# Kernel tuning notes

Hardware: AMD Instinct MI355X
Metric: run time of the kernel (lower is better)

## Reference

```python
import jax, jax.numpy as jnp
import numpy as np

D_MODEL = 1024
NUM_HEADS = 16
D_K = D_MODEL // NUM_HEADS
B, S = 2, 2048


def setup_inputs() -> dict:
    key = jax.random.key(0)
    ks = jax.random.split(key, 4)
    scale = 1.0 / np.sqrt(D_MODEL)
    x = jax.random.normal(ks[0], (B, S, D_MODEL), dtype=jnp.float32)
    w_qkv = jax.random.normal(ks[1], (D_MODEL, 3 * D_MODEL), dtype=jnp.float32) * scale
    b_qkv = jnp.zeros((3 * D_MODEL,), dtype=jnp.float32)
    w_out = jax.random.normal(ks[2], (D_MODEL, D_MODEL), dtype=jnp.float32) * scale
    b_out = jnp.zeros((D_MODEL,), dtype=jnp.float32)
    # causal mask: 1 where attention is allowed (j <= i), 0 elsewhere
    mask = jnp.tril(jnp.ones((S, S), dtype=jnp.int32))
    return {"x": x, "mask": mask, "w_qkv": w_qkv, "b_qkv": b_qkv,
            "w_out": w_out, "b_out": b_out}


def reference(x, mask, w_qkv, b_qkv, w_out, b_out):
    Bb, Ss, C = x.shape
    qkv = x @ w_qkv + b_qkv                      # [B,S,3C]
    q, k, v = jnp.split(qkv, 3, axis=-1)
    def split_heads(t):
        return t.reshape(Bb, Ss, NUM_HEADS, D_K).transpose(0, 2, 1, 3)  # [B,H,S,Dk]
    q, k, v = split_heads(q), split_heads(k), split_heads(v)
    scores = jnp.einsum('bhqd,bhkd->bhqk', q, k) / jnp.sqrt(jnp.float32(D_K))
    scores = jnp.where(mask == 0, -jnp.inf, scores)
    weights = jax.nn.softmax(scores, axis=-1)
    weights = jnp.nan_to_num(weights, nan=0.0)   # matches torch.nan_to_num
    attn = jnp.einsum('bhqk,bhkd->bhqd', weights, v)
    attn = attn.transpose(0, 2, 1, 3).reshape(Bb, Ss, C)
    return attn @ w_out + b_out
```

## Files before the change

kernel.cpp:

```cpp
#include <hip/hip_runtime.h>
#include <hip/hip_bf16.h>

#define D_MODEL 1024
#define NUM_HEADS 16
#define D_K 64
#define BATCH 2
#define SEQ 2048

typedef __attribute__((ext_vector_type(8))) short bf16x8;
typedef __attribute__((ext_vector_type(4))) float f32x4;

union P16 { int4 i4; ushort u[8]; };
union FU { float f; unsigned int u; };

__device__ __forceinline__ float bf2f(ushort u) {
    union { unsigned int i; float f; } c; c.i = ((unsigned int)u) << 16; return c.f;
}
__device__ __forceinline__ ushort f2bf(float f) {
    union { float f; unsigned int i; } c; c.f = f;
    unsigned int x = c.i;
    return (ushort)((x + 0x7fff + ((x >> 16) & 1)) >> 16);
}

__device__ __forceinline__ bool wave_detect_f32(const ushort* x) {
    ushort u = x[2 * (threadIdx.x & 63)];
    int e = (u >> 7) & 0xFF;
    unsigned long long bl = __ballot(e >= 100 && e <= 141);
    return __popcll(bl) < 32;
}

__global__ __launch_bounds__(256)
void prep_all(const ushort* __restrict__ x, const void* __restrict__ Wq,
              const void* __restrict__ Wo, ushort* __restrict__ xb,
              ushort* __restrict__ WqT, ushort* __restrict__ WoT,
              int* __restrict__ flag)
{
    const bool f32 = wave_detect_f32(x);
    const int bx = blockIdx.x, tx = threadIdx.x;
    if (bx == 0 && tx == 0) flag[0] = f32 ? 1 : 0;

    if (bx >= 1024) {
        if (!f32) return;
        int i = ((bx - 1024) * 256 + tx) * 8;
        const float* f = (const float*)x + i;
        float4 a = *(const float4*)f, b = *(const float4*)(f + 4);
        P16 r;
        r.u[0] = f2bf(a.x); r.u[1] = f2bf(a.y); r.u[2] = f2bf(a.z); r.u[3] = f2bf(a.w);
        r.u[4] = f2bf(b.x); r.u[5] = f2bf(b.y); r.u[6] = f2bf(b.z); r.u[7] = f2bf(b.w);
        *(int4*)(xb + i) = r.i4;
        return;
    }

    __shared__ ushort t[64][72];
    const int nb = bx & 63, kb = bx >> 6;
    const void* W; ushort* WT; int N, n0;
    if (nb < 48) { W = Wq; WT = WqT; N = 3 * D_MODEL; n0 = nb * 64; }
    else         { W = Wo; WT = WoT; N = D_MODEL;     n0 = (nb - 48) * 64; }
    const int k0 = kb * 64, K = D_MODEL;
    #pragma unroll
    for (int p = 0; p < 16; ++p) {
        int r = p * 4 + (tx >> 6), c = tx & 63;
        float v = f32 ? ((const float*)W)[(size_t)(k0 + r) * N + n0 + c]
                      : bf2f(((const ushort*)W)[(size_t)(k0 + r) * N + n0 + c]);
        t[r][c] = f2bf(v);
    }
    __syncthreads();
    #pragma unroll
    for (int p = 0; p < 16; ++p) {
        int nn = p * 4 + (tx >> 6), kk = tx & 63;
        WT[(size_t)(n0 + nn) * K + k0 + kk] = t[kk][nn];
    }
}

template<int MODE>
__global__ __launch_bounds__(256)
void gemm128(const void* __restrict__ Araw, const ushort* __restrict__ Aconv,
             const ushort* __restrict__ WT, const void* __restrict__ bias,
             void* __restrict__ out, int N, int K, const int* __restrict__ flag)
{
    __shared__ ushort As[2][128 * 32];
    __shared__ ushort Bs[2][128 * 32];

    const int f = *flag;
    const ushort* A = (MODE == 1) ? (f ? Aconv : (const ushort*)Araw) : Aconv;

    const int tid = threadIdx.x;
    const int w = tid >> 6, lane = tid & 63;
    const int ln = lane & 15, quad = lane >> 4;
    const int m0 = blockIdx.y * 128, n0 = blockIdx.x * 128;
    const int wm = (w >> 1) * 64, wn = (w & 1) * 64;

    const int s0 = w * 128 + lane, s1 = s0 + 64;
    const int ar0 = s0 >> 2, ak0 = ((s0 & 3) ^ ((ar0 >> 1) & 3)) * 8;
    const int ar1 = s1 >> 2, ak1 = ((s1 & 3) ^ ((ar1 >> 1) & 3)) * 8;
    const size_t aoff0 = (size_t)(m0 + ar0) * K + ak0;
    const size_t aoff1 = (size_t)(m0 + ar1) * K + ak1;
    const size_t boff0 = (size_t)(n0 + ar0) * K + ak0;
    const size_t boff1 = (size_t)(n0 + ar1) * K + ak1;

    const int physc = (quad ^ ((ln >> 1) & 3)) * 8;

    f32x4 acc[4][4] = {};

    const int nk = K >> 5;
    int4 a0 = *(const int4*)(A + aoff0);
    int4 a1 = *(const int4*)(A + aoff1);
    int4 b0 = *(const int4*)(WT + boff0);
    int4 b1 = *(const int4*)(WT + boff1);
    *(int4*)(As[0] + s0 * 8) = a0;
    *(int4*)(As[0] + s1 * 8) = a1;
    *(int4*)(Bs[0] + s0 * 8) = b0;
    *(int4*)(Bs[0] + s1 * 8) = b1;
    a0 = *(const int4*)(A + aoff0 + 32);
    a1 = *(const int4*)(A + aoff1 + 32);
    b0 = *(const int4*)(WT + boff0 + 32);
    b1 = *(const int4*)(WT + boff1 + 32);
    __syncthreads();

    for (int kt = 0; kt < nk; ++kt) {
        const int cur = kt & 1;
        if (kt + 1 < nk) {
            *(int4*)(As[1 - cur] + s0 * 8) = a0;
            *(int4*)(As[1 - cur] + s1 * 8) = a1;
            *(int4*)(Bs[1 - cur] + s0 * 8) = b0;
            *(int4*)(Bs[1 - cur] + s1 * 8) = b1;
        }
        if (kt + 2 < nk) {
            const int kc = (kt + 2) * 32;
            a0 = *(const int4*)(A + aoff0 + kc);
            a1 = *(const int4*)(A + aoff1 + kc);
            b0 = *(const int4*)(WT + boff0 + kc);
            b1 = *(const int4*)(WT + boff1 + kc);
        }

        bf16x8 af[4], bf[4];
        #pragma unroll
        for (int t = 0; t < 4; ++t) {
            af[t] = *(const bf16x8*)(As[cur] + (wm + t * 16 + ln) * 32 + physc);
            bf[t] = *(const bf16x8*)(Bs[cur] + (wn + t * 16 + ln) * 32 + physc);
        }
        #pragma unroll
        for (int mi = 0; mi < 4; ++mi)
            #pragma unroll
            for (int ni = 0; ni < 4; ++ni)
                acc[mi][ni] = __builtin_amdgcn_mfma_f32_16x16x32_bf16(
                    af[mi], bf[ni], acc[mi][ni], 0, 0, 0);
        __syncthreads();
    }

    #pragma unroll
    for (int mi = 0; mi < 4; ++mi) {
        #pragma unroll
        for (int ni = 0; ni < 4; ++ni) {
            int col = n0 + wn + ni * 16 + ln;
            float bb = f ? ((const float*)bias)[col] : bf2f(((const ushort*)bias)[col]);
            #pragma unroll
            for (int r = 0; r < 4; ++r) {
                int row = m0 + wm + mi * 16 + quad * 4 + r;
                float v = acc[mi][ni][r] + bb;
                if (MODE == 0 && f) ((float*)out)[(size_t)row * N + col] = v;
                else                ((ushort*)out)[(size_t)row * N + col] = f2bf(v);
            }
        }
    }
}

template<int MODE>
__global__ __launch_bounds__(256)
void gemm64(const void* __restrict__ Araw, const ushort* __restrict__ Aconv,
            const ushort* __restrict__ WT, const void* __restrict__ bias,
            void* __restrict__ out, int N, int K, const int* __restrict__ flag)
{
    __shared__ ushort As[2][64 * 32];
    __shared__ ushort Bs[2][128 * 32];

    const int f = *flag;
    const ushort* A = (MODE == 1) ? (f ? Aconv : (const ushort*)Araw) : Aconv;

    const int tid = threadIdx.x;
    const int w = tid >> 6, lane = tid & 63;
    const int ln = lane & 15, quad = lane >> 4;
    const int m0 = blockIdx.y * 64, n0 = blockIdx.x * 128;
    const int wn = w * 32;

    const int sa = tid;
    const int arow = sa >> 2, akc = ((sa & 3) ^ ((arow >> 1) & 3)) * 8;
    const size_t aoff = (size_t)(m0 + arow) * K + akc;
    const int sb0 = tid, sb1 = tid + 256;
    const int br0 = sb0 >> 2, bk0 = ((sb0 & 3) ^ ((br0 >> 1) & 3)) * 8;
    const int br1 = sb1 >> 2, bk1 = ((sb1 & 3) ^ ((br1 >> 1) & 3)) * 8;
    const size_t boff0 = (size_t)(n0 + br0) * K + bk0;
    const size_t boff1 = (size_t)(n0 + br1) * K + bk1;

    const int physc = (quad ^ ((ln >> 1) & 3)) * 8;

    f32x4 acc[4][2] = {};

    const int nk = K >> 5;
    int4 a0 = *(const int4*)(A + aoff);
    int4 b0 = *(const int4*)(WT + boff0);
    int4 b1 = *(const int4*)(WT + boff1);
    *(int4*)(As[0] + sa * 8)  = a0;
    *(int4*)(Bs[0] + sb0 * 8) = b0;
    *(int4*)(Bs[0] + sb1 * 8) = b1;
    a0 = *(const int4*)(A + aoff + 32);
    b0 = *(const int4*)(WT + boff0 + 32);
    b1 = *(const int4*)(WT + boff1 + 32);
    __syncthreads();

    for (int kt = 0; kt < nk; ++kt) {
        const int cur = kt & 1;
        if (kt + 1 < nk) {
            *(int4*)(As[1 - cur] + sa * 8)  = a0;
            *(int4*)(Bs[1 - cur] + sb0 * 8) = b0;
            *(int4*)(Bs[1 - cur] + sb1 * 8) = b1;
        }
        if (kt + 2 < nk) {
            const int kc = (kt + 2) * 32;
            a0 = *(const int4*)(A + aoff + kc);
            b0 = *(const int4*)(WT + boff0 + kc);
            b1 = *(const int4*)(WT + boff1 + kc);
        }

        bf16x8 af[4], bf[2];
        #pragma unroll
        for (int t = 0; t < 4; ++t)
            af[t] = *(const bf16x8*)(As[cur] + (t * 16 + ln) * 32 + physc);
        #pragma unroll
        for (int t = 0; t < 2; ++t)
            bf[t] = *(const bf16x8*)(Bs[cur] + (wn + t * 16 + ln) * 32 + physc);
        #pragma unroll
        for (int mi = 0; mi < 4; ++mi)
            #pragma unroll
            for (int ni = 0; ni < 2; ++ni)
                acc[mi][ni] = __builtin_amdgcn_mfma_f32_16x16x32_bf16(
                    af[mi], bf[ni], acc[mi][ni], 0, 0, 0);
        __syncthreads();
    }

    #pragma unroll
    for (int mi = 0; mi < 4; ++mi) {
        #pragma unroll
        for (int ni = 0; ni < 2; ++ni) {
            int col = n0 + wn + ni * 16 + ln;
            float bb = f ? ((const float*)bias)[col] : bf2f(((const ushort*)bias)[col]);
            #pragma unroll
            for (int r = 0; r < 4; ++r) {
                int row = m0 + mi * 16 + quad * 4 + r;
                float v = acc[mi][ni][r] + bb;
                if (MODE == 0 && f) ((float*)out)[(size_t)row * N + col] = v;
                else                ((ushort*)out)[(size_t)row * N + col] = f2bf(v);
            }
        }
    }
}

__global__ __launch_bounds__(256)
void flash_attn7(const ushort* __restrict__ qkv, ushort* __restrict__ attn)
{
    __shared__ ushort Ks[64][72];
    __shared__ ushort Vs[64][72];
    __shared__ ushort QPs[128][72];

    const int tid  = threadIdx.x;
    const int wave = tid >> 6, lane = tid & 63;
    const int ln   = lane & 15, quad = lane >> 4;
    const int pg   = wave >> 1, ww = wave & 1;
    const int bh   = blockIdx.x;
    const int ky   = blockIdx.y;
    const int k    = (ky < 8) ? ky : 23 - ky;
    const int xx   = 2 * k + pg;
    const int b    = bh >> 4, hh = bh & (NUM_HEADS - 1);
    const int W3   = 3 * D_MODEL;
    const size_t hbase = (size_t)b * SEQ * W3 + hh * D_K;

    const int q0A = 32 * (63 - xx), q0B = 32 * xx;
    const int ntA = 32 - k, ntB = k + 1;

    const int qrr = tid >> 1, qcol = (tid & 1) * 32;
    const int ksr = tid >> 2, ksc = (tid & 3) * 16;
    const int vp  = tid & 31, vg = (tid >> 5) * 8;

    {
        const int qpg = qrr >> 6, qmt = (qrr >> 5) & 1, ql = qrr & 31;
        const int qxx = 2 * k + qpg;
        const int grow = qmt ? (32 * qxx + ql) : (32 * (63 - qxx) + ql);
        const ushort* src = qkv + hbase + (size_t)grow * W3 + qcol;
        #pragma unroll
        for (int h = 0; h < 4; ++h) {
            P16 v; v.i4 = *(const int4*)(src + h * 8);
            #pragma unroll
            for (int e = 0; e < 8; ++e) v.u[e] = f2bf(bf2f(v.u[e]) * 0.18033688011f);
            *(int4*)(&QPs[qrr][qcol + h * 8]) = v.i4;
        }
    }
    __syncthreads();
    bf16x8 qf[2][2];
    #pragma unroll
    for (int mt = 0; mt < 2; ++mt)
        #pragma unroll
        for (int s = 0; s < 2; ++s)
            qf[mt][s] = *(const bf16x8*)(&QPs[pg * 64 + mt * 32 + ww * 16 + ln][s * 32 + quad * 8]);

    f32x4 acc_o[2][4] = {};
    f32x4 acc_l[2] = {};

    bf16x8 ones8;
    #pragma unroll
    for (int e = 0; e < 8; ++e) ones8[e] = (short)0x3F80;

    const ushort* Kbase = qkv + hbase + D_MODEL;
    const ushort* Vbase = qkv + hbase + 2 * D_MODEL;

    int4 kreg[2], vreg[2];
    {
        const ushort* ksrc = Kbase + (size_t)ksr * W3 + ksc;
        kreg[0] = *(const int4*)(ksrc);
        kreg[1] = *(const int4*)(ksrc + 8);
        vreg[0] = *(const int4*)(Vbase + (size_t)(2 * vp)     * W3 + vg);
        vreg[1] = *(const int4*)(Vbase + (size_t)(2 * vp + 1) * W3 + vg);
    }

    for (int jt = 0; jt < ntA; ++jt) {
        const int j0 = jt * 64;
        const bool doB = (jt < ntB);
        __syncthreads();

        *(int4*)(&Ks[ksr][ksc])     = kreg[0];
        *(int4*)(&Ks[ksr][ksc + 8]) = kreg[1];
        {
            P16 v0, v1; v0.i4 = vreg[0]; v1.i4 = vreg[1];
            #pragma unroll
            for (int e = 0; e < 8; ++e) {
                unsigned int pack = (unsigned int)v0.u[e] | ((unsigned int)v1.u[e] << 16);
                *(unsigned int*)(&Vs[vg + e][2 * vp]) = pack;
            }
        }
        __syncthreads();

        if (jt + 1 < ntA) {
            const int jn = j0 + 64;
            const ushort* ksrc = Kbase + (size_t)(jn + ksr) * W3 + ksc;
            kreg[0] = *(const int4*)(ksrc);
            kreg[1] = *(const int4*)(ksrc + 8);
            vreg[0] = *(const int4*)(Vbase + (size_t)(jn + 2 * vp)     * W3 + vg);
            vreg[1] = *(const int4*)(Vbase + (size_t)(jn + 2 * vp + 1) * W3 + vg);
        }

        f32x4 sa[2][4];
        #pragma unroll
        for (int t = 0; t < 4; ++t) {
            bf16x8 k0 = *(const bf16x8*)(&Ks[t * 16 + ln][quad * 8]);
            bf16x8 k1 = *(const bf16x8*)(&Ks[t * 16 + ln][32 + quad * 8]);
            {
                f32x4 z = {};
                z = __builtin_amdgcn_mfma_f32_16x16x32_bf16(qf[0][0], k0, z, 0, 0, 0);
                z = __builtin_amdgcn_mfma_f32_16x16x32_bf16(qf[0][1], k1, z, 0, 0, 0);
                sa[0][t] = z;
            }
            if (doB) {
                f32x4 z = {};
                z = __builtin_amdgcn_mfma_f32_16x16x32_bf16(qf[1][0], k0, z, 0, 0, 0);
                z = __builtin_amdgcn_mfma_f32_16x16x32_bf16(qf[1][1], k1, z, 0, 0, 0);
                sa[1][t] = z;
            }
        }

        if (jt == ntA - 1) {
            const int rowb = q0A + ww * 16 + quad * 4;
            #pragma unroll
            for (int t = 0; t < 4; ++t)
                #pragma unroll
                for (int r = 0; r < 4; ++r)
                    if (j0 + t * 16 + ln > rowb + r) sa[0][t][r] = -1e30f;
        }
        if (doB && jt == ntB - 1) {
            const int rowb = q0B + ww * 16 + quad * 4;
            #pragma unroll
            for (int t = 0; t < 4; ++t)
                #pragma unroll
                for (int r = 0; r < 4; ++r)
                    if (j0 + t * 16 + ln > rowb + r) sa[1][t][r] = -1e30f;
        }

        const int lnx = ln ^ ((quad & 1) * 8);
        #pragma unroll
        for (int mt = 0; mt < 2; ++mt) {
            if (mt && !doB) break;
            #pragma unroll
            for (int r = 0; r < 4; ++r) {
                const int prow = pg * 64 + mt * 32 + ww * 16 + quad * 4 + r;
                #pragma unroll
                for (int t = 0; t < 4; ++t) {
                    FU cc; cc.f = exp2f(sa[mt][t][r]);
                    QPs[prow][((t ^ (quad >> 1)) * 16) + lnx] = (ushort)(cc.u >> 16);
                }
            }
        }

        #pragma unroll
        for (int s = 0; s < 2; ++s) {
            const int pcol = s * 32 + ((quad ^ ((ln >> 2) & 3)) * 8);
            bf16x8 pf0 = *(const bf16x8*)(&QPs[pg * 64 + ww * 16 + ln][pcol]);
            bf16x8 pf1;
            if (doB) pf1 = *(const bf16x8*)(&QPs[pg * 64 + 32 + ww * 16 + ln][pcol]);
            #pragma unroll
            for (int t = 0; t < 4; ++t) {
                bf16x8 vf = *(const bf16x8*)(&Vs[t * 16 + ln][s * 32 + quad * 8]);
                acc_o[0][t] = __builtin_amdgcn_mfma_f32_16x16x32_bf16(pf0, vf, acc_o[0][t], 0, 0, 0);
                if (doB)
                    acc_o[1][t] = __builtin_amdgcn_mfma_f32_16x16x32_bf16(pf1, vf, acc_o[1][t], 0, 0, 0);
            }
            acc_l[0] = __builtin_amdgcn_mfma_f32_16x16x32_bf16(pf0, ones8, acc_l[0], 0, 0, 0);
            if (doB)
                acc_l[1] = __builtin_amdgcn_mfma_f32_16x16x32_bf16(pf1, ones8, acc_l[1], 0, 0, 0);
        }
    }

    #pragma unroll
    for (int mt = 0; mt < 2; ++mt) {
        const int q0 = mt ? q0B : q0A;
        #pragma unroll
        for (int r = 0; r < 4; ++r) {
            float inv = 1.0f / acc_l[mt][r];
            int i = q0 + ww * 16 + quad * 4 + r;
            size_t rowoff = ((size_t)(b * SEQ + i)) * D_MODEL + hh * D_K;
            #pragma unroll
            for (int t = 0; t < 4; ++t)
                attn[rowoff + t * 16 + ln] = f2bf(acc_o[mt][t][r] * inv);
        }
    }
}

extern "C" void kernel_launch(void* const* d_in, const int* in_sizes, int n_in,
                              void* d_out, int out_size, void* d_ws, size_t ws_size,
                              hipStream_t stream)
{
    const void* x     = d_in[0];
    const void* w_qkv = d_in[2];
    const void* b_qkv = d_in[3];
    const void* w_out = d_in[4];
    const void* b_out = d_in[5];

    char* ws = (char*)d_ws;
    int*    flag   = (int*)ws;                  size_t off = 256;
    ushort* WqkvT  = (ushort*)(ws + off);       off += (size_t)3 * D_MODEL * D_MODEL * 2;
    ushort* WoutT  = (ushort*)(ws + off);       off += (size_t)D_MODEL * D_MODEL * 2;
    ushort* qkv_ws = (ushort*)(ws + off);       off += (size_t)BATCH * SEQ * 3 * D_MODEL * 2;
    ushort* xb     = (ushort*)(ws + off);
    ushort* attn_ws = xb;

    const int M = BATCH * SEQ;

    prep_all<<<3072, 256, 0, stream>>>((const ushort*)x, w_qkv, w_out,
                                       xb, WqkvT, WoutT, flag);

    gemm128<1><<<dim3(3 * D_MODEL / 128, M / 128), 256, 0, stream>>>(
        x, xb, WqkvT, b_qkv, qkv_ws, 3 * D_MODEL, D_MODEL, flag);

    dim3 ga(BATCH * NUM_HEADS, 16);
    flash_attn7<<<ga, 256, 0, stream>>>(qkv_ws, attn_ws);

    gemm64<0><<<dim3(D_MODEL / 128, M / 64), 256, 0, stream>>>(
        attn_ws, attn_ws, WoutT, b_out, d_out, D_MODEL, D_MODEL, flag);
}
```

Before: 214.2 us.

## Split attention key tiles across wave pairs and double the attention grid

Each attention block now handles one pair of query tiles rather than two. Its four waves split each 64-key tile so that each wave pair computes half of the score columns and the matching half of the PV products. The partial output and row-sum accumulators are reduced through shared memory at the end. This doubles the number of blocks, aiming for better occupancy and load spread across CUs, and it adds a final cross-wave reduction plus extra barriers.

```diff
diff --git a/kernel.cpp b/kernel.cpp
--- a/kernel.cpp
+++ b/kernel.cpp
@@ -256,38 +256,36 @@
 }
 
 __global__ __launch_bounds__(256)
-void flash_attn7(const ushort* __restrict__ qkv, ushort* __restrict__ attn)
+void flash_attn8(const ushort* __restrict__ qkv, ushort* __restrict__ attn)
 {
-    __shared__ ushort Ks[64][72];
-    __shared__ ushort Vs[64][72];
-    __shared__ ushort QPs[128][72];
+    __shared__ ushort SMEM[3 * 64 * 72];
+    ushort (*Ks)[72]  = (ushort(*)[72])(SMEM);
+    ushort (*Vs)[72]  = (ushort(*)[72])(SMEM + 64 * 72);
+    ushort (*QPs)[72] = (ushort(*)[72])(SMEM + 2 * 64 * 72);
 
     const int tid  = threadIdx.x;
     const int wave = tid >> 6, lane = tid & 63;
     const int ln   = lane & 15, quad = lane >> 4;
-    const int pg   = wave >> 1, ww = wave & 1;
+    const int ww   = wave & 1;
+    const int kw   = wave >> 1;
     const int bh   = blockIdx.x;
-    const int ky   = blockIdx.y;
-    const int k    = (ky < 8) ? ky : 23 - ky;
-    const int xx   = 2 * k + pg;
+    const int xx   = blockIdx.y;
     const int b    = bh >> 4, hh = bh & (NUM_HEADS - 1);
     const int W3   = 3 * D_MODEL;
     const size_t hbase = (size_t)b * SEQ * W3 + hh * D_K;
 
     const int q0A = 32 * (63 - xx), q0B = 32 * xx;
-    const int ntA = 32 - k, ntB = k + 1;
-
-    const int qrr = tid >> 1, qcol = (tid & 1) * 32;
+    const int ntA = (65 - xx) >> 1, ntB = (xx + 2) >> 1;
+
     const int ksr = tid >> 2, ksc = (tid & 3) * 16;
     const int vp  = tid & 31, vg = (tid >> 5) * 8;
 
     {
-        const int qpg = qrr >> 6, qmt = (qrr >> 5) & 1, ql = qrr & 31;
-        const int qxx = 2 * k + qpg;
-        const int grow = qmt ? (32 * qxx + ql) : (32 * (63 - qxx) + ql);
+        const int qrr = tid >> 2, qcol = (tid & 3) * 16;
+        const int grow = (qrr < 32) ? (q0A + qrr) : (q0B + (qrr - 32));
         const ushort* src = qkv + hbase + (size_t)grow * W3 + qcol;
         #pragma unroll
-        for (int h = 0; h < 4; ++h) {
+        for (int h = 0; h < 2; ++h) {
             P16 v; v.i4 = *(const int4*)(src + h * 8);
             #pragma unroll
             for (int e = 0; e < 8; ++e) v.u[e] = f2bf(bf2f(v.u[e]) * 0.18033688011f);
@@ -300,7 +298,7 @@
     for (int mt = 0; mt < 2; ++mt)
         #pragma unroll
         for (int s = 0; s < 2; ++s)
-            qf[mt][s] = *(const bf16x8*)(&QPs[pg * 64 + mt * 32 + ww * 16 + ln][s * 32 + quad * 8]);
+            qf[mt][s] = *(const bf16x8*)(&QPs[mt * 32 + ww * 16 + ln][s * 32 + quad * 8]);
 
     f32x4 acc_o[2][4] = {};
     f32x4 acc_l[2] = {};
@@ -347,40 +345,41 @@
             vreg[1] = *(const int4*)(Vbase + (size_t)(jn + 2 * vp + 1) * W3 + vg);
         }
 
-        f32x4 sa[2][4];
-        #pragma unroll
-        for (int t = 0; t < 4; ++t) {
+        f32x4 sa[2][2];
+        #pragma unroll
+        for (int tt = 0; tt < 2; ++tt) {
+            const int t = 2 * kw + tt;
             bf16x8 k0 = *(const bf16x8*)(&Ks[t * 16 + ln][quad * 8]);
             bf16x8 k1 = *(const bf16x8*)(&Ks[t * 16 + ln][32 + quad * 8]);
             {
                 f32x4 z = {};
                 z = __builtin_amdgcn_mfma_f32_16x16x32_bf16(qf[0][0], k0, z, 0, 0, 0);
                 z = __builtin_amdgcn_mfma_f32_16x16x32_bf16(qf[0][1], k1, z, 0, 0, 0);
-                sa[0][t] = z;
+                sa[0][tt] = z;
             }
             if (doB) {
                 f32x4 z = {};
                 z = __builtin_amdgcn_mfma_f32_16x16x32_bf16(qf[1][0], k0, z, 0, 0, 0);
                 z = __builtin_amdgcn_mfma_f32_16x16x32_bf16(qf[1][1], k1, z, 0, 0, 0);
-                sa[1][t] = z;
+                sa[1][tt] = z;
             }
         }
 
         if (jt == ntA - 1) {
             const int rowb = q0A + ww * 16 + quad * 4;
             #pragma unroll
-            for (int t = 0; t < 4; ++t)
+            for (int tt = 0; tt < 2; ++tt)
                 #pragma unroll
                 for (int r = 0; r < 4; ++r)
-                    if (j0 + t * 16 + ln > rowb + r) sa[0][t][r] = -1e30f;
+                    if (j0 + (2 * kw + tt) * 16 + ln > rowb + r) sa[0][tt][r] = -1e30f;
         }
         if (doB && jt == ntB - 1) {
             const int rowb = q0B + ww * 16 + quad * 4;
             #pragma unroll
-            for (int t = 0; t < 4; ++t)
+            for (int tt = 0; tt < 2; ++tt)
                 #pragma unroll
                 for (int r = 0; r < 4; ++r)
-                    if (j0 + t * 16 + ln > rowb + r) sa[1][t][r] = -1e30f;
+                    if (j0 + (2 * kw + tt) * 16 + ln > rowb + r) sa[1][tt][r] = -1e30f;
         }
 
         const int lnx = ln ^ ((quad & 1) * 8);
@@ -389,21 +388,22 @@
             if (mt && !doB) break;
             #pragma unroll
             for (int r = 0; r < 4; ++r) {
-                const int prow = pg * 64 + mt * 32 + ww * 16 + quad * 4 + r;
-                #pragma unroll
-                for (int t = 0; t < 4; ++t) {
-                    FU cc; cc.f = exp2f(sa[mt][t][r]);
+                const int prow = mt * 32 + ww * 16 + quad * 4 + r;
+                #pragma unroll
+                for (int tt = 0; tt < 2; ++tt) {
+                    const int t = 2 * kw + tt;
+                    FU cc; cc.f = exp2f(sa[mt][tt][r]);
                     QPs[prow][((t ^ (quad >> 1)) * 16) + lnx] = (ushort)(cc.u >> 16);
                 }
             }
         }
 
-        #pragma unroll
-        for (int s = 0; s < 2; ++s) {
+        {
+            const int s = kw;
             const int pcol = s * 32 + ((quad ^ ((ln >> 2) & 3)) * 8);
-            bf16x8 pf0 = *(const bf16x8*)(&QPs[pg * 64 + ww * 16 + ln][pcol]);
+            bf16x8 pf0 = *(const bf16x8*)(&QPs[ww * 16 + ln][pcol]);
             bf16x8 pf1;
-            if (doB) pf1 = *(const bf16x8*)(&QPs[pg * 64 + 32 + ww * 16 + ln][pcol]);
+            if (doB) pf1 = *(const bf16x8*)(&QPs[32 + ww * 16 + ln][pcol]);
             #pragma unroll
             for (int t = 0; t < 4; ++t) {
                 bf16x8 vf = *(const bf16x8*)(&Vs[t * 16 + ln][s * 32 + quad * 8]);
@@ -417,17 +417,49 @@
         }
     }
 
-    #pragma unroll
-    for (int mt = 0; mt < 2; ++mt) {
-        const int q0 = mt ? q0B : q0A;
-        #pragma unroll
-        for (int r = 0; r < 4; ++r) {
-            float inv = 1.0f / acc_l[mt][r];
-            int i = q0 + ww * 16 + quad * 4 + r;
-            size_t rowoff = ((size_t)(b * SEQ + i)) * D_MODEL + hh * D_K;
+    __syncthreads();
+    float* red = (float*)SMEM;
+    if (kw == 1) {
+        float* dst = red + (ww * 64 + lane) * 41;
+        int idx = 0;
+        #pragma unroll
+        for (int mt = 0; mt < 2; ++mt)
             #pragma unroll
             for (int t = 0; t < 4; ++t)
-                attn[rowoff + t * 16 + ln] = f2bf(acc_o[mt][t][r] * inv);
+                #pragma unroll
+                for (int r = 0; r < 4; ++r) dst[idx++] = acc_o[mt][t][r];
+        #pragma unroll
+        for (int mt = 0; mt < 2; ++mt)
+            #pragma unroll
+            for (int r = 0; r < 4; ++r) dst[32 + mt * 4 + r] = acc_l[mt][r];
+    }
+    __syncthreads();
+    if (kw == 0) {
+        const float* src = red + (ww * 64 + lane) * 41;
+        int idx = 0;
+        #pragma unroll
+        for (int mt = 0; mt < 2; ++mt)
+            #pragma unroll
+            for (int t = 0; t < 4; ++t)
+                #pragma unroll
+                for (int r = 0; r < 4; ++r) acc_o[mt][t][r] += src[idx++];
+        #pragma unroll
+        for (int mt = 0; mt < 2; ++mt)
+            #pragma unroll
+            for (int r = 0; r < 4; ++r) acc_l[mt][r] += src[32 + mt * 4 + r];
+
+        #pragma unroll
+        for (int mt = 0; mt < 2; ++mt) {
+            const int q0 = mt ? q0B : q0A;
+            #pragma unroll
+            for (int r = 0; r < 4; ++r) {
+                float inv = 1.0f / acc_l[mt][r];
+                int i = q0 + ww * 16 + quad * 4 + r;
+                size_t rowoff = ((size_t)(b * SEQ + i)) * D_MODEL + hh * D_K;
+                #pragma unroll
+                for (int t = 0; t < 4; ++t)
+                    attn[rowoff + t * 16 + ln] = f2bf(acc_o[mt][t][r] * inv);
+            }
         }
     }
 }
@@ -458,8 +490,8 @@
     gemm128<1><<<dim3(3 * D_MODEL / 128, M / 128), 256, 0, stream>>>(
         x, xb, WqkvT, b_qkv, qkv_ws, 3 * D_MODEL, D_MODEL, flag);
 
-    dim3 ga(BATCH * NUM_HEADS, 16);
-    flash_attn7<<<ga, 256, 0, stream>>>(qkv_ws, attn_ws);
+    dim3 ga(BATCH * NUM_HEADS, 32);
+    flash_attn8<<<ga, 256, 0, stream>>>(qkv_ws, attn_ws);
 
     gemm64<0><<<dim3(D_MODEL / 128, M / 64), 256, 0, stream>>>(
         attn_ws, attn_ws, WoutT, b_out, d_out, D_MODEL, D_MODEL, flag);
```

Result: slower. 249.7 us (+16.6%).

## Double-buffer K/V tiles in LDS in the flash attention loop

Applied to the files above, without the earlier changes.

The attention kernel now keeps two LDS buffers for the K and V tiles. Tile 0 is written before the loop, and each iteration stores the next tile into the other buffer while computing on the current one. Global loads are issued two tiles ahead. This cuts the barriers per key tile from two to one, so LDS stores can overlap the MFMA work. The cost is more shared memory (about 55KB per block) and an extra prologue.

```diff
diff --git a/kernel.cpp b/kernel.cpp
--- a/kernel.cpp
+++ b/kernel.cpp
@@ -256,10 +256,10 @@
 }
 
 __global__ __launch_bounds__(256)
-void flash_attn7(const ushort* __restrict__ qkv, ushort* __restrict__ attn)
+void flash_attn9(const ushort* __restrict__ qkv, ushort* __restrict__ attn)
 {
-    __shared__ ushort Ks[64][72];
-    __shared__ ushort Vs[64][72];
+    __shared__ ushort Ks[2][64][72];
+    __shared__ ushort Vs[2][64][72];
     __shared__ ushort QPs[128][72];
 
     const int tid  = threadIdx.x;
@@ -320,26 +320,42 @@
         vreg[0] = *(const int4*)(Vbase + (size_t)(2 * vp)     * W3 + vg);
         vreg[1] = *(const int4*)(Vbase + (size_t)(2 * vp + 1) * W3 + vg);
     }
+    *(int4*)(&Ks[0][ksr][ksc])     = kreg[0];
+    *(int4*)(&Ks[0][ksr][ksc + 8]) = kreg[1];
+    {
+        P16 v0, v1; v0.i4 = vreg[0]; v1.i4 = vreg[1];
+        #pragma unroll
+        for (int e = 0; e < 8; ++e) {
+            unsigned int pack = (unsigned int)v0.u[e] | ((unsigned int)v1.u[e] << 16);
+            *(unsigned int*)(&Vs[0][vg + e][2 * vp]) = pack;
+        }
+    }
+    if (ntA > 1) {
+        const ushort* ksrc = Kbase + (size_t)(64 + ksr) * W3 + ksc;
+        kreg[0] = *(const int4*)(ksrc);
+        kreg[1] = *(const int4*)(ksrc + 8);
+        vreg[0] = *(const int4*)(Vbase + (size_t)(64 + 2 * vp)     * W3 + vg);
+        vreg[1] = *(const int4*)(Vbase + (size_t)(64 + 2 * vp + 1) * W3 + vg);
+    }
+    __syncthreads();
 
     for (int jt = 0; jt < ntA; ++jt) {
+        const int cur = jt & 1;
         const int j0 = jt * 64;
         const bool doB = (jt < ntB);
-        __syncthreads();
-
-        *(int4*)(&Ks[ksr][ksc])     = kreg[0];
-        *(int4*)(&Ks[ksr][ksc + 8]) = kreg[1];
-        {
+
+        if (jt + 1 < ntA) {
+            *(int4*)(&Ks[1 - cur][ksr][ksc])     = kreg[0];
+            *(int4*)(&Ks[1 - cur][ksr][ksc + 8]) = kreg[1];
             P16 v0, v1; v0.i4 = vreg[0]; v1.i4 = vreg[1];
             #pragma unroll
             for (int e = 0; e < 8; ++e) {
                 unsigned int pack = (unsigned int)v0.u[e] | ((unsigned int)v1.u[e] << 16);
-                *(unsigned int*)(&Vs[vg + e][2 * vp]) = pack;
-            }
-        }
-        __syncthreads();
-
-        if (jt + 1 < ntA) {
-            const int jn = j0 + 64;
+                *(unsigned int*)(&Vs[1 - cur][vg + e][2 * vp]) = pack;
+            }
+        }
+        if (jt + 2 < ntA) {
+            const int jn = j0 + 128;
             const ushort* ksrc = Kbase + (size_t)(jn + ksr) * W3 + ksc;
             kreg[0] = *(const int4*)(ksrc);
             kreg[1] = *(const int4*)(ksrc + 8);
@@ -350,8 +366,8 @@
         f32x4 sa[2][4];
         #pragma unroll
         for (int t = 0; t < 4; ++t) {
-            bf16x8 k0 = *(const bf16x8*)(&Ks[t * 16 + ln][quad * 8]);
-            bf16x8 k1 = *(const bf16x8*)(&Ks[t * 16 + ln][32 + quad * 8]);
+            bf16x8 k0 = *(const bf16x8*)(&Ks[cur][t * 16 + ln][quad * 8]);
+            bf16x8 k1 = *(const bf16x8*)(&Ks[cur][t * 16 + ln][32 + quad * 8]);
             {
                 f32x4 z = {};
                 z = __builtin_amdgcn_mfma_f32_16x16x32_bf16(qf[0][0], k0, z, 0, 0, 0);
@@ -406,7 +422,7 @@
             if (doB) pf1 = *(const bf16x8*)(&QPs[pg * 64 + 32 + ww * 16 + ln][pcol]);
             #pragma unroll
             for (int t = 0; t < 4; ++t) {
-                bf16x8 vf = *(const bf16x8*)(&Vs[t * 16 + ln][s * 32 + quad * 8]);
+                bf16x8 vf = *(const bf16x8*)(&Vs[cur][t * 16 + ln][s * 32 + quad * 8]);
                 acc_o[0][t] = __builtin_amdgcn_mfma_f32_16x16x32_bf16(pf0, vf, acc_o[0][t], 0, 0, 0);
                 if (doB)
                     acc_o[1][t] = __builtin_amdgcn_mfma_f32_16x16x32_bf16(pf1, vf, acc_o[1][t], 0, 0, 0);
@@ -415,6 +431,8 @@
             if (doB)
                 acc_l[1] = __builtin_amdgcn_mfma_f32_16x16x32_bf16(pf1, ones8, acc_l[1], 0, 0, 0);
         }
+
+        __syncthreads();
     }
 
     #pragma unroll
@@ -459,7 +477,7 @@
         x, xb, WqkvT, b_qkv, qkv_ws, 3 * D_MODEL, D_MODEL, flag);
 
     dim3 ga(BATCH * NUM_HEADS, 16);
-    flash_attn7<<<ga, 256, 0, stream>>>(qkv_ws, attn_ws);
+    flash_attn9<<<ga, 256, 0, stream>>>(qkv_ws, attn_ws);
 
     gemm64<0><<<dim3(D_MODEL / 128, M / 64), 256, 0, stream>>>(
         attn_ws, attn_ws, WoutT, b_out, d_out, D_MODEL, D_MODEL, flag);
```

Result: slower. 220.9 us (+3.2%).

## Split attention KV loop across two blocks and merge partials in output GEMM

Applied to the files above, without the earlier changes.

Attention now launches twice as many blocks. Each handles alternating KV tiles for its query rows and writes unnormalized fp32 partial outputs and row sums to workspace. The output projection GEMM reads both partials, adds them, normalizes, converts to bf16 while loading its A tiles, then multiplies. This raises parallelism in the attention stage and drops its normalization epilogue, at the cost of extra fp32 workspace traffic and a fallback path when the workspace is too small.

```diff
diff --git a/kernel.cpp b/kernel.cpp
--- a/kernel.cpp
+++ b/kernel.cpp
@@ -168,6 +168,7 @@
 template<int MODE>
 __global__ __launch_bounds__(256)
 void gemm64(const void* __restrict__ Araw, const ushort* __restrict__ Aconv,
+            const float* __restrict__ pL,
             const ushort* __restrict__ WT, const void* __restrict__ bias,
             void* __restrict__ out, int N, int K, const int* __restrict__ flag)
 {
@@ -175,7 +176,11 @@
     __shared__ ushort Bs[2][128 * 32];
 
     const int f = *flag;
-    const ushort* A = (MODE == 1) ? (f ? Aconv : (const ushort*)Araw) : Aconv;
+    const ushort* A = (MODE == 1) ? (f ? Aconv : (const ushort*)Araw)
+                                  : (const ushort*)Aconv;
+    const float* PO = (const float*)Araw;
+    constexpr size_t HALF_O = (size_t)BATCH * SEQ * D_MODEL;
+    constexpr size_t HALF_L = (size_t)BATCH * SEQ * NUM_HEADS;
 
     const int tid = threadIdx.x;
     const int w = tid >> 6, lane = tid & 63;
@@ -186,6 +191,7 @@
     const int sa = tid;
     const int arow = sa >> 2, akc = ((sa & 3) ^ ((arow >> 1) & 3)) * 8;
     const size_t aoff = (size_t)(m0 + arow) * K + akc;
+    const int rowl = (m0 + arow) * NUM_HEADS;
     const int sb0 = tid, sb1 = tid + 256;
     const int br0 = sb0 >> 2, bk0 = ((sb0 & 3) ^ ((br0 >> 1) & 3)) * 8;
     const int br1 = sb1 >> 2, bk1 = ((sb1 & 3) ^ ((br1 >> 1) & 3)) * 8;
@@ -197,13 +203,45 @@
     f32x4 acc[4][2] = {};
 
     const int nk = K >> 5;
-    int4 a0 = *(const int4*)(A + aoff);
+    int4 a0;
+    float4 ax0, ax1, ay0, ay1;
+
+    auto cvtA = [&](int ktile) -> int4 {
+        float il = 1.0f / (pL[rowl + (ktile >> 1)] + pL[HALF_L + rowl + (ktile >> 1)]);
+        P16 r;
+        r.u[0] = f2bf((ax0.x + ay0.x) * il);
+        r.u[1] = f2bf((ax0.y + ay0.y) * il);
+        r.u[2] = f2bf((ax0.z + ay0.z) * il);
+        r.u[3] = f2bf((ax0.w + ay0.w) * il);
+        r.u[4] = f2bf((ax1.x + ay1.x) * il);
+        r.u[5] = f2bf((ax1.y + ay1.y) * il);
+        r.u[6] = f2bf((ax1.z + ay1.z) * il);
+        r.u[7] = f2bf((ax1.w + ay1.w) * il);
+        return r.i4;
+    };
+
+    if constexpr (MODE == 2) {
+        ax0 = *(const float4*)(PO + aoff);
+        ax1 = *(const float4*)(PO + aoff + 4);
+        ay0 = *(const float4*)(PO + HALF_O + aoff);
+        ay1 = *(const float4*)(PO + HALF_O + aoff + 4);
+    } else {
+        a0 = *(const int4*)(A + aoff);
+    }
     int4 b0 = *(const int4*)(WT + boff0);
     int4 b1 = *(const int4*)(WT + boff1);
-    *(int4*)(As[0] + sa * 8)  = a0;
+    if constexpr (MODE == 2) *(int4*)(As[0] + sa * 8) = cvtA(0);
+    else                     *(int4*)(As[0] + sa * 8) = a0;
     *(int4*)(Bs[0] + sb0 * 8) = b0;
     *(int4*)(Bs[0] + sb1 * 8) = b1;
-    a0 = *(const int4*)(A + aoff + 32);
+    if constexpr (MODE == 2) {
+        ax0 = *(const float4*)(PO + aoff + 32);
+        ax1 = *(const float4*)(PO + aoff + 36);
+        ay0 = *(const float4*)(PO + HALF_O + aoff + 32);
+        ay1 = *(const float4*)(PO + HALF_O + aoff + 36);
+    } else {
+        a0 = *(const int4*)(A + aoff + 32);
+    }
     b0 = *(const int4*)(WT + boff0 + 32);
     b1 = *(const int4*)(WT + boff1 + 32);
     __syncthreads();
@@ -211,13 +249,21 @@
     for (int kt = 0; kt < nk; ++kt) {
         const int cur = kt & 1;
         if (kt + 1 < nk) {
-            *(int4*)(As[1 - cur] + sa * 8)  = a0;
+            if constexpr (MODE == 2) *(int4*)(As[1 - cur] + sa * 8) = cvtA(kt + 1);
+            else                     *(int4*)(As[1 - cur] + sa * 8) = a0;
             *(int4*)(Bs[1 - cur] + sb0 * 8) = b0;
             *(int4*)(Bs[1 - cur] + sb1 * 8) = b1;
         }
         if (kt + 2 < nk) {
             const int kc = (kt + 2) * 32;
-            a0 = *(const int4*)(A + aoff + kc);
+            if constexpr (MODE == 2) {
+                ax0 = *(const float4*)(PO + aoff + kc);
+                ax1 = *(const float4*)(PO + aoff + kc + 4);
+                ay0 = *(const float4*)(PO + HALF_O + aoff + kc);
+                ay1 = *(const float4*)(PO + HALF_O + aoff + kc + 4);
+            } else {
+                a0 = *(const int4*)(A + aoff + kc);
+            }
             b0 = *(const int4*)(WT + boff0 + kc);
             b1 = *(const int4*)(WT + boff1 + kc);
         }
@@ -248,7 +294,7 @@
             for (int r = 0; r < 4; ++r) {
                 int row = m0 + mi * 16 + quad * 4 + r;
                 float v = acc[mi][ni][r] + bb;
-                if (MODE == 0 && f) ((float*)out)[(size_t)row * N + col] = v;
+                if (MODE != 1 && f) ((float*)out)[(size_t)row * N + col] = v;
                 else                ((ushort*)out)[(size_t)row * N + col] = f2bf(v);
             }
         }
@@ -432,6 +478,189 @@
     }
 }
 
+__global__ __launch_bounds__(256)
+void flash_attn10(const ushort* __restrict__ qkv, float* __restrict__ pO,
+                  float* __restrict__ pL)
+{
+    __shared__ ushort Ks[64][72];
+    __shared__ ushort Vs[64][72];
+    __shared__ ushort QPs[128][72];
+
+    const int tid  = threadIdx.x;
+    const int wave = tid >> 6, lane = tid & 63;
+    const int ln   = lane & 15, quad = lane >> 4;
+    const int pg   = wave >> 1, ww = wave & 1;
+    const int bh   = blockIdx.x;
+    const int yy   = blockIdx.y;
+    const int ky   = yy >> 1, half = yy & 1;
+    const int k    = (ky < 8) ? ky : 23 - ky;
+    const int xx   = 2 * k + pg;
+    const int b    = bh >> 4, hh = bh & (NUM_HEADS - 1);
+    const int W3   = 3 * D_MODEL;
+    const size_t hbase = (size_t)b * SEQ * W3 + hh * D_K;
+
+    const int q0A = 32 * (63 - xx), q0B = 32 * xx;
+    const int ntA = 32 - k, ntB = k + 1;
+
+    const int qrr = tid >> 1, qcol = (tid & 1) * 32;
+    const int ksr = tid >> 2, ksc = (tid & 3) * 16;
+    const int vp  = tid & 31, vg = (tid >> 5) * 8;
+
+    {
+        const int qpg = qrr >> 6, qmt = (qrr >> 5) & 1, ql = qrr & 31;
+        const int qxx = 2 * k + qpg;
+        const int grow = qmt ? (32 * qxx + ql) : (32 * (63 - qxx) + ql);
+        const ushort* src = qkv + hbase + (size_t)grow * W3 + qcol;
+        #pragma unroll
+        for (int h = 0; h < 4; ++h) {
+            P16 v; v.i4 = *(const int4*)(src + h * 8);
+            #pragma unroll
+            for (int e = 0; e < 8; ++e) v.u[e] = f2bf(bf2f(v.u[e]) * 0.18033688011f);
+            *(int4*)(&QPs[qrr][qcol + h * 8]) = v.i4;
+        }
+    }
+    __syncthreads();
+    bf16x8 qf[2][2];
+    #pragma unroll
+    for (int mt = 0; mt < 2; ++mt)
+        #pragma unroll
+        for (int s = 0; s < 2; ++s)
+            qf[mt][s] = *(const bf16x8*)(&QPs[pg * 64 + mt * 32 + ww * 16 + ln][s * 32 + quad * 8]);
+
+    f32x4 acc_o[2][4] = {};
+    f32x4 acc_l[2] = {};
+
+    bf16x8 ones8;
+    #pragma unroll
+    for (int e = 0; e < 8; ++e) ones8[e] = (short)0x3F80;
+
+    const ushort* Kbase = qkv + hbase + D_MODEL;
+    const ushort* Vbase = qkv + hbase + 2 * D_MODEL;
+
+    int4 kreg[2], vreg[2];
+    {
+        const int jf = half * 64;
+        const ushort* ksrc = Kbase + (size_t)(jf + ksr) * W3 + ksc;
+        kreg[0] = *(const int4*)(ksrc);
+        kreg[1] = *(const int4*)(ksrc + 8);
+        vreg[0] = *(const int4*)(Vbase + (size_t)(jf + 2 * vp)     * W3 + vg);
+        vreg[1] = *(const int4*)(Vbase + (size_t)(jf + 2 * vp + 1) * W3 + vg);
+    }
+
+    for (int jt = half; jt < ntA; jt += 2) {
+        const int j0 = jt * 64;
+        const bool doB = (jt < ntB);
+        __syncthreads();
+
+        *(int4*)(&Ks[ksr][ksc])     = kreg[0];
+        *(int4*)(&Ks[ksr][ksc + 8]) = kreg[1];
+        {
+            P16 v0, v1; v0.i4 = vreg[0]; v1.i4 = vreg[1];
+            #pragma unroll
+            for (int e = 0; e < 8; ++e) {
+                unsigned int pack = (unsigned int)v0.u[e] | ((unsigned int)v1.u[e] << 16);
+                *(unsigned int*)(&Vs[vg + e][2 * vp]) = pack;
+            }
+        }
+        __syncthreads();
+
+        if (jt + 2 < ntA) {
+            const int jn = j0 + 128;
+            const ushort* ksrc = Kbase + (size_t)(jn + ksr) * W3 + ksc;
+            kreg[0] = *(const int4*)(ksrc);
+            kreg[1] = *(const int4*)(ksrc + 8);
+            vreg[0] = *(const int4*)(Vbase + (size_t)(jn + 2 * vp)     * W3 + vg);
+            vreg[1] = *(const int4*)(Vbase + (size_t)(jn + 2 * vp + 1) * W3 + vg);
+        }
+
+        f32x4 sa[2][4];
+        #pragma unroll
+        for (int t = 0; t < 4; ++t) {
+            bf16x8 k0 = *(const bf16x8*)(&Ks[t * 16 + ln][quad * 8]);
+            bf16x8 k1 = *(const bf16x8*)(&Ks[t * 16 + ln][32 + quad * 8]);
+            {
+                f32x4 z = {};
+                z = __builtin_amdgcn_mfma_f32_16x16x32_bf16(qf[0][0], k0, z, 0, 0, 0);
+                z = __builtin_amdgcn_mfma_f32_16x16x32_bf16(qf[0][1], k1, z, 0, 0, 0);
+                sa[0][t] = z;
+            }
+            if (doB) {
+                f32x4 z = {};
+                z = __builtin_amdgcn_mfma_f32_16x16x32_bf16(qf[1][0], k0, z, 0, 0, 0);
+                z = __builtin_amdgcn_mfma_f32_16x16x32_bf16(qf[1][1], k1, z, 0, 0, 0);
+                sa[1][t] = z;
+            }
+        }
+
+        if (jt == ntA - 1) {
+            const int rowb = q0A + ww * 16 + quad * 4;
+            #pragma unroll
+            for (int t = 0; t < 4; ++t)
+                #pragma unroll
+                for (int r = 0; r < 4; ++r)
+                    if (j0 + t * 16 + ln > rowb + r) sa[0][t][r] = -1e30f;
+        }
+        if (doB && jt == ntB - 1) {
+            const int rowb = q0B + ww * 16 + quad * 4;
+            #pragma unroll
+            for (int t = 0; t < 4; ++t)
+                #pragma unroll
+                for (int r = 0; r < 4; ++r)
+                    if (j0 + t * 16 + ln > rowb + r) sa[1][t][r] = -1e30f;
+        }
+
+        const int lnx = ln ^ ((quad & 1) * 8);
+        #pragma unroll
+        for (int mt = 0; mt < 2; ++mt) {
+            if (mt && !doB) break;
+            #pragma unroll
+            for (int r = 0; r < 4; ++r) {
+                const int prow = pg * 64 + mt * 32 + ww * 16 + quad * 4 + r;
+                #pragma unroll
+                for (int t = 0; t < 4; ++t) {
+                    FU cc; cc.f = exp2f(sa[mt][t][r]);
+                    QPs[prow][((t ^ (quad >> 1)) * 16) + lnx] = (ushort)(cc.u >> 16);
+                }
+            }
+        }
+
+        #pragma unroll
+        for (int s = 0; s < 2; ++s) {
+            const int pcol = s * 32 + ((quad ^ ((ln >> 2) & 3)) * 8);
+            bf16x8 pf0 = *(const bf16x8*)(&QPs[pg * 64 + ww * 16 + ln][pcol]);
+            bf16x8 pf1;
+            if (doB) pf1 = *(const bf16x8*)(&QPs[pg * 64 + 32 + ww * 16 + ln][pcol]);
+            #pragma unroll
+            for (int t = 0; t < 4; ++t) {
+                bf16x8 vf = *(const bf16x8*)(&Vs[t * 16 + ln][s * 32 + quad * 8]);
+                acc_o[0][t] = __builtin_amdgcn_mfma_f32_16x16x32_bf16(pf0, vf, acc_o[0][t], 0, 0, 0);
+                if (doB)
+                    acc_o[1][t] = __builtin_amdgcn_mfma_f32_16x16x32_bf16(pf1, vf, acc_o[1][t], 0, 0, 0);
+            }
+            acc_l[0] = __builtin_amdgcn_mfma_f32_16x16x32_bf16(pf0, ones8, acc_l[0], 0, 0, 0);
+            if (doB)
+                acc_l[1] = __builtin_amdgcn_mfma_f32_16x16x32_bf16(pf1, ones8, acc_l[1], 0, 0, 0);
+        }
+    }
+
+    const size_t oH = (size_t)half * BATCH * SEQ * D_MODEL;
+    const size_t lH = (size_t)half * BATCH * SEQ * NUM_HEADS;
+    #pragma unroll
+    for (int mt = 0; mt < 2; ++mt) {
+        const int q0 = mt ? q0B : q0A;
+        #pragma unroll
+        for (int r = 0; r < 4; ++r) {
+            int i = q0 + ww * 16 + quad * 4 + r;
+            size_t rowoff = ((size_t)(b * SEQ + i)) * D_MODEL + hh * D_K;
+            #pragma unroll
+            for (int t = 0; t < 4; ++t)
+                pO[oH + rowoff + t * 16 + ln] = acc_o[mt][t][r];
+            if (ln == 0)
+                pL[lH + (size_t)(b * SEQ + i) * NUM_HEADS + hh] = acc_l[mt][r];
+        }
+    }
+}
+
 extern "C" void kernel_launch(void* const* d_in, const int* in_sizes, int n_in,
                               void* d_out, int out_size, void* d_ws, size_t ws_size,
                               hipStream_t stream)
@@ -447,8 +676,15 @@
     ushort* WqkvT  = (ushort*)(ws + off);       off += (size_t)3 * D_MODEL * D_MODEL * 2;
     ushort* WoutT  = (ushort*)(ws + off);       off += (size_t)D_MODEL * D_MODEL * 2;
     ushort* qkv_ws = (ushort*)(ws + off);       off += (size_t)BATCH * SEQ * 3 * D_MODEL * 2;
-    ushort* xb     = (ushort*)(ws + off);
+    char*   share  = ws + off;
+    ushort* xb     = (ushort*)share;
     ushort* attn_ws = xb;
+    float*  pO     = (float*)share;
+    const size_t pO_bytes = (size_t)2 * BATCH * SEQ * D_MODEL * 4;
+    float*  pL     = (float*)(share + pO_bytes);
+    const size_t pL_bytes = (size_t)2 * BATCH * SEQ * NUM_HEADS * 4;
+    const size_t need_split = off + pO_bytes + pL_bytes;
+    const bool use_split = ws_size >= need_split;
 
     const int M = BATCH * SEQ;
 
@@ -458,9 +694,15 @@
     gemm128<1><<<dim3(3 * D_MODEL / 128, M / 128), 256, 0, stream>>>(
         x, xb, WqkvT, b_qkv, qkv_ws, 3 * D_MODEL, D_MODEL, flag);
 
-    dim3 ga(BATCH * NUM_HEADS, 16);
-    flash_attn7<<<ga, 256, 0, stream>>>(qkv_ws, attn_ws);
-
-    gemm64<0><<<dim3(D_MODEL / 128, M / 64), 256, 0, stream>>>(
-        attn_ws, attn_ws, WoutT, b_out, d_out, D_MODEL, D_MODEL, flag);
-}
+    if (use_split) {
+        dim3 ga(BATCH * NUM_HEADS, 32);
+        flash_attn10<<<ga, 256, 0, stream>>>(qkv_ws, pO, pL);
+        gemm64<2><<<dim3(D_MODEL / 128, M / 64), 256, 0, stream>>>(
+            pO, nullptr, pL, WoutT, b_out, d_out, D_MODEL, D_MODEL, flag);
+    } else {
+        dim3 ga(BATCH * NUM_HEADS, 16);
+        flash_attn7<<<ga, 256, 0, stream>>>(qkv_ws, attn_ws);
+        gemm64<0><<<dim3(D_MODEL / 128, M / 64), 256, 0, stream>>>(
+            attn_ws, attn_ws, nullptr, WoutT, b_out, d_out, D_MODEL, D_MODEL, flag);
+    }
+}
```

Measured after the change: 241.0 us. 1.13x slower.
